# Performance work log

Hardware: AMD Instinct MI355X
Metric: run time of the kernel (lower is better)

Reference implementation:

```python
import jax, jax.numpy as jnp
import numpy as np

DIM = 768
NUM_HEADS = 12
HEAD_DIM = DIM // NUM_HEADS
SCALE = HEAD_DIM ** -0.5


def setup_inputs() -> dict:
    key = jax.random.key(0)
    k_x, k_qkv, k_proj, k_pb = jax.random.split(key, 4)
    B, N = 8, 1024
    x = jax.random.normal(k_x, (B, N, DIM), dtype=jnp.float32)
    # nn.Linear(dim, 3*dim, bias=False): weight [3*dim, dim]
    w_qkv = jax.random.normal(k_qkv, (3 * DIM, DIM), dtype=jnp.float32) * (DIM ** -0.5)
    # nn.Linear(dim, dim): weight [dim, dim], bias [dim]
    w_proj = jax.random.normal(k_proj, (DIM, DIM), dtype=jnp.float32) * (DIM ** -0.5)
    b_proj = jax.random.normal(k_pb, (DIM,), dtype=jnp.float32) * 0.01
    return {"x": x, "w_qkv": w_qkv, "w_proj": w_proj, "b_proj": b_proj}


def reference(x, w_qkv, w_proj, b_proj):
    B, N, C = x.shape
    H, D = NUM_HEADS, HEAD_DIM
    # qkv: [B, N, 3C] -> [3, B, H, N, D]
    qkv = jnp.einsum('bnc,oc->bno', x, w_qkv)
    qkv = qkv.reshape(B, N, 3, H, D).transpose(2, 0, 3, 1, 4)
    q, k, v = qkv[0], qkv[1], qkv[2]
    # scores in float32 (module explicitly casts to float)
    attn = jnp.einsum('bhnd,bhmd->bhnm', q.astype(jnp.float32), k.astype(jnp.float32)) * SCALE
    attn = jax.nn.softmax(attn, axis=-1)
    attn = jnp.where(jnp.isnan(attn), 0.0, attn)  # masked_fill nan -> 0
    out = jnp.einsum('bhnm,bhmd->bhnd', attn, v.astype(jnp.float32))
    out = out.transpose(0, 2, 1, 3).reshape(B, N, C)
    out = jnp.einsum('bnc,oc->bno', out, w_proj) + b_proj
    return out
```

## Files before the change

kernel.cpp:

```cpp
#include <hip/hip_runtime.h>

typedef _Float16 half8 __attribute__((ext_vector_type(8)));
typedef _Float16 half4 __attribute__((ext_vector_type(4)));
typedef float f32x4 __attribute__((ext_vector_type(4)));

#define NHEAD 12
#define HDIM  64
#define SEQ   1024
#define CDIM  768
#define O3    2304
#define MTOK  8192

__device__ __forceinline__ void load_lds16(const void* g, void* l) {
  __builtin_amdgcn_global_load_lds(
      (const __attribute__((address_space(1))) unsigned int*)g,
      (__attribute__((address_space(3))) unsigned int*)l, 16, 0, 0);
}

__global__ __launch_bounds__(256) void cast_f2h(const float* __restrict__ in,
                                                _Float16* __restrict__ out) {
  size_t i = ((size_t)blockIdx.x * 256 + threadIdx.x) * 4;
  float4 v = *reinterpret_cast<const float4*>(in + i);
  half4 h;
  h[0] = (_Float16)v.x; h[1] = (_Float16)v.y; h[2] = (_Float16)v.z; h[3] = (_Float16)v.w;
  *reinterpret_cast<half4*>(out + i) = h;
}

__global__ __launch_bounds__(256) void qkv_gemm(const _Float16* __restrict__ A,
                                                const _Float16* __restrict__ Bw,
                                                _Float16* __restrict__ Qh,
                                                _Float16* __restrict__ Kh,
                                                _Float16* __restrict__ VT) {
  __shared__ _Float16 As0[128 * 64], Bs0[128 * 64];
  __shared__ _Float16 As1[128 * 64], Bs1[128 * 64];
  const int tid  = threadIdx.x;
  const int lane = tid & 63;
  const int wv   = tid >> 6;
  const int wm   = wv >> 1;
  const int wn   = wv & 1;
  const int fr   = lane & 15;
  const int kg   = lane >> 4;

  const int lin = blockIdx.y * gridDim.x + blockIdx.x;
  const int cpx = (gridDim.x * gridDim.y) >> 3;
  const int swz = (lin & 7) * cpx + (lin >> 3);
  const int m0  = (swz / 18) * 128;
  const int n0  = (swz % 18) * 128;

  f32x4 acc[4][4];
#pragma unroll
  for (int i = 0; i < 4; ++i)
#pragma unroll
    for (int j = 0; j < 4; ++j) acc[i][j] = (f32x4){0.f, 0.f, 0.f, 0.f};

  auto stage = [&](_Float16* Ad, _Float16* Bd, int kt) {
#pragma unroll
    for (int r = 0; r < 4; ++r) {
      const int c = r * 256 + tid;
      const int row = c >> 3, cc = c & 7;
      load_lds16(A + (size_t)(m0 + row) * CDIM + kt + ((cc ^ (row & 7)) * 8), Ad + c * 8);
    }
#pragma unroll
    for (int r = 0; r < 4; ++r) {
      const int c = r * 256 + tid;
      const int row = c >> 3, cc = c & 7;
      load_lds16(Bw + (size_t)(n0 + row) * CDIM + kt + ((cc ^ (row & 7)) * 8), Bd + c * 8);
    }
  };

  auto compute = [&](const _Float16* As, const _Float16* Bs) {
#pragma unroll
    for (int kk = 0; kk < 2; ++kk) {
      half8 a[4], b[4];
#pragma unroll
      for (int i = 0; i < 4; ++i) {
        const int row = wm * 64 + i * 16 + fr;
        a[i] = *reinterpret_cast<const half8*>(
            &As[row * 64 + (((kk * 4 + kg) ^ (row & 7)) * 8)]);
      }
#pragma unroll
      for (int j = 0; j < 4; ++j) {
        const int row = wn * 64 + j * 16 + fr;
        b[j] = *reinterpret_cast<const half8*>(
            &Bs[row * 64 + (((kk * 4 + kg) ^ (row & 7)) * 8)]);
      }
#pragma unroll
      for (int i = 0; i < 4; ++i)
#pragma unroll
        for (int j = 0; j < 4; ++j)
          acc[i][j] = __builtin_amdgcn_mfma_f32_16x16x32_f16(a[i], b[j], acc[i][j], 0, 0, 0);
    }
  };

  stage(As0, Bs0, 0);
  __syncthreads();
  for (int it = 0; it < 6; ++it) {
    const int kt = it * 128;
    stage(As1, Bs1, kt + 64);
    compute(As0, Bs0);
    __syncthreads();
    if (kt + 128 < CDIM) stage(As0, Bs0, kt + 128);
    compute(As1, Bs1);
    __syncthreads();
  }

  const int t     = n0 / CDIM;
  const int hbase = n0 - t * CDIM;
#pragma unroll
  for (int i = 0; i < 4; ++i) {
    const int mrow = m0 + wm * 64 + i * 16 + kg * 4;
#pragma unroll
    for (int j = 0; j < 4; ++j) {
      const int hd = hbase + wn * 64 + j * 16 + fr;
      const int h  = hd >> 6, d = hd & 63;
#pragma unroll
      for (int r = 0; r < 4; ++r) {
        const int m  = mrow + r;
        const int bb = m >> 10, nn = m & 1023;
        const float v = acc[i][j][r];
        if (t == 0)
          Qh[(((size_t)(bb * NHEAD + h)) << 16) + (nn << 6) + d] = (_Float16)(v * 0.125f);
        else if (t == 1)
          Kh[(((size_t)(bb * NHEAD + h)) << 16) + (nn << 6) + d] = (_Float16)v;
        else
          VT[(((size_t)(bb * NHEAD + h)) << 16) + (d << 10) + nn] = (_Float16)v;
      }
    }
  }
}

__global__ __launch_bounds__(256) void attn_kernel(const _Float16* __restrict__ Qh,
                                                   const _Float16* __restrict__ Kh,
                                                   const _Float16* __restrict__ VT,
                                                   _Float16* __restrict__ AO) {
  __shared__ _Float16 Ks0[64 * 64], Vs0[64 * 64];
  __shared__ _Float16 Ks1[64 * 64], Vs1[64 * 64];
  __shared__ _Float16 Ps[4 * 16 * 64];
  const int tid  = threadIdx.x;
  const int lane = tid & 63;
  const int w    = tid >> 6;
  const int fr   = lane & 15;
  const int kg   = lane >> 4;
  const int kh   = kg * 8;
  const int bh   = blockIdx.x;
  const int qt   = blockIdx.y;
  const int q0   = qt * 64 + w * 16;
  const size_t qkbase = (size_t)bh * SEQ * HDIM;
  char* const psw = (char*)&Ps[w * 16 * 64];

  half8 qb[2];
#pragma unroll
  for (int ks = 0; ks < 2; ++ks)
    qb[ks] = *reinterpret_cast<const half8*>(
        &Qh[qkbase + (size_t)(q0 + fr) * HDIM + ks * 32 + kh]);

  f32x4 O[4];
  float mrun = -__builtin_inff();
  float lrun = 0.f;
#pragma unroll
  for (int fd = 0; fd < 4; ++fd) O[fd] = (f32x4){0.f, 0.f, 0.f, 0.f};

  auto stageKV = [&](_Float16* Kd, _Float16* Vd, int kt) {
#pragma unroll
    for (int r = 0; r < 2; ++r) {
      const int c = r * 256 + tid;
      const int row = c >> 3, cc = c & 7;
      load_lds16(&Kh[qkbase + (size_t)(kt + row) * HDIM + ((cc ^ (row & 7)) * 8)], Kd + c * 8);
    }
#pragma unroll
    for (int r = 0; r < 2; ++r) {
      const int c = r * 256 + tid;
      const int row = c >> 3, cc = c & 7;
      load_lds16(&VT[(size_t)bh * HDIM * SEQ + (size_t)row * SEQ + kt + ((cc ^ (row & 7)) * 8)],
                 Vd + c * 8);
    }
  };

  auto computeKV = [&](const _Float16* Ksrc, const _Float16* Vsrc) {
    f32x4 st[4];
#pragma unroll
    for (int fc = 0; fc < 4; ++fc) st[fc] = (f32x4){0.f, 0.f, 0.f, 0.f};
#pragma unroll
    for (int ks = 0; ks < 2; ++ks) {
#pragma unroll
      for (int fc = 0; fc < 4; ++fc) {
        const int row = fc * 16 + fr;
        const int colh = ks * 32 + kh;
        half8 ka = *reinterpret_cast<const half8*>(
            &Ksrc[row * 64 + (((colh >> 3) ^ (row & 7)) << 3)]);
        st[fc] = __builtin_amdgcn_mfma_f32_16x16x32_f16(ka, qb[ks], st[fc], 0, 0, 0);
      }
    }

    float mx = st[0][0];
#pragma unroll
    for (int fc = 0; fc < 4; ++fc)
#pragma unroll
      for (int r = 0; r < 4; ++r) mx = fmaxf(mx, st[fc][r]);
    mx = fmaxf(mx, __shfl_xor(mx, 16));
    mx = fmaxf(mx, __shfl_xor(mx, 32));
    const float mnew = fmaxf(mrun, mx);
    const float corr = __expf(mrun - mnew);
    mrun = mnew;
    float rs = 0.f;
#pragma unroll
    for (int fc = 0; fc < 4; ++fc)
#pragma unroll
      for (int r = 0; r < 4; ++r) {
        const float p = __expf(st[fc][r] - mnew);
        st[fc][r] = p;
        rs += p;
      }
    rs += __shfl_xor(rs, 16);
    rs += __shfl_xor(rs, 32);
    lrun = lrun * corr + rs;

#pragma unroll
    for (int r = 0; r < 4; ++r) {
      const float c4 = __shfl(corr, kg * 4 + r);
#pragma unroll
      for (int fd = 0; fd < 4; ++fd) O[fd][r] *= c4;
    }

#pragma unroll
    for (int fc = 0; fc < 4; ++fc) {
      half4 pk;
      pk[0] = (_Float16)st[fc][0];
      pk[1] = (_Float16)st[fc][1];
      pk[2] = (_Float16)st[fc][2];
      pk[3] = (_Float16)st[fc][3];
      const int slot = (fc * 2 + (kg >> 1)) ^ (fr & 7);
      *reinterpret_cast<half4*>(psw + fr * 128 + slot * 16 + (kg & 1) * 8) = pk;
    }

#pragma unroll
    for (int ks = 0; ks < 2; ++ks) {
      const int rslot = (ks * 4 + kg) ^ (fr & 7);
      half8 pa = *reinterpret_cast<half8*>(psw + fr * 128 + rslot * 16);
#pragma unroll
      for (int fd = 0; fd < 4; ++fd) {
        const int row = fd * 16 + fr;
        const int colh = ks * 32 + kh;
        half8 vb = *reinterpret_cast<const half8*>(
            &Vsrc[row * 64 + (((colh >> 3) ^ (row & 7)) << 3)]);
        O[fd] = __builtin_amdgcn_mfma_f32_16x16x32_f16(pa, vb, O[fd], 0, 0, 0);
      }
    }
  };

  stageKV(Ks0, Vs0, 0);
  __syncthreads();
  for (int it = 0; it < 8; ++it) {
    const int kt = it * 128;
    stageKV(Ks1, Vs1, kt + 64);
    computeKV(Ks0, Vs0);
    __syncthreads();
    if (kt + 128 < SEQ) stageKV(Ks0, Vs0, kt + 128);
    computeKV(Ks1, Vs1);
    __syncthreads();
  }

  const int b = bh / NHEAD, h = bh % NHEAD;
  const float linv = 1.0f / lrun;
#pragma unroll
  for (int r = 0; r < 4; ++r) {
    const float lq = __shfl(linv, kg * 4 + r);
    const int n = q0 + kg * 4 + r;
#pragma unroll
    for (int fd = 0; fd < 4; ++fd)
      AO[((size_t)b * SEQ + n) * CDIM + h * HDIM + fd * 16 + fr] =
          (_Float16)(O[fd][r] * lq);
  }
}

__global__ __launch_bounds__(256) void proj_gemm(const _Float16* __restrict__ A,
                                                 const _Float16* __restrict__ Bw,
                                                 const float* __restrict__ bias,
                                                 float* __restrict__ Out) {
  __shared__ _Float16 As0[128 * 64], Bs0[128 * 64];
  __shared__ _Float16 As1[128 * 64], Bs1[128 * 64];
  const int tid  = threadIdx.x;
  const int lane = tid & 63;
  const int wv   = tid >> 6;
  const int wm   = wv >> 1;
  const int wn   = wv & 1;
  const int fr   = lane & 15;
  const int kg   = lane >> 4;

  const int lin = blockIdx.y * gridDim.x + blockIdx.x;
  const int cpx = (gridDim.x * gridDim.y) >> 3;
  const int swz = (lin & 7) * cpx + (lin >> 3);
  const int m0  = (swz / 6) * 128;
  const int n0  = (swz % 6) * 128;

  f32x4 acc[4][4];
#pragma unroll
  for (int i = 0; i < 4; ++i)
#pragma unroll
    for (int j = 0; j < 4; ++j) acc[i][j] = (f32x4){0.f, 0.f, 0.f, 0.f};

  auto stage = [&](_Float16* Ad, _Float16* Bd, int kt) {
#pragma unroll
    for (int r = 0; r < 4; ++r) {
      const int c = r * 256 + tid;
      const int row = c >> 3, cc = c & 7;
      load_lds16(A + (size_t)(m0 + row) * CDIM + kt + ((cc ^ (row & 7)) * 8), Ad + c * 8);
    }
#pragma unroll
    for (int r = 0; r < 4; ++r) {
      const int c = r * 256 + tid;
      const int row = c >> 3, cc = c & 7;
      load_lds16(Bw + (size_t)(n0 + row) * CDIM + kt + ((cc ^ (row & 7)) * 8), Bd + c * 8);
    }
  };

  auto compute = [&](const _Float16* As, const _Float16* Bs) {
#pragma unroll
    for (int kk = 0; kk < 2; ++kk) {
      half8 a[4], b[4];
#pragma unroll
      for (int i = 0; i < 4; ++i) {
        const int row = wm * 64 + i * 16 + fr;
        a[i] = *reinterpret_cast<const half8*>(
            &As[row * 64 + (((kk * 4 + kg) ^ (row & 7)) * 8)]);
      }
#pragma unroll
      for (int j = 0; j < 4; ++j) {
        const int row = wn * 64 + j * 16 + fr;
        b[j] = *reinterpret_cast<const half8*>(
            &Bs[row * 64 + (((kk * 4 + kg) ^ (row & 7)) * 8)]);
      }
#pragma unroll
      for (int i = 0; i < 4; ++i)
#pragma unroll
        for (int j = 0; j < 4; ++j)
          acc[i][j] = __builtin_amdgcn_mfma_f32_16x16x32_f16(a[i], b[j], acc[i][j], 0, 0, 0);
    }
  };

  stage(As0, Bs0, 0);
  __syncthreads();
  for (int it = 0; it < 6; ++it) {
    const int kt = it * 128;
    stage(As1, Bs1, kt + 64);
    compute(As0, Bs0);
    __syncthreads();
    if (kt + 128 < CDIM) stage(As0, Bs0, kt + 128);
    compute(As1, Bs1);
    __syncthreads();
  }

#pragma unroll
  for (int i = 0; i < 4; ++i) {
    const int mrow = m0 + wm * 64 + i * 16 + kg * 4;
#pragma unroll
    for (int j = 0; j < 4; ++j) {
      const int ocol = n0 + wn * 64 + j * 16 + fr;
      const float bv = bias[ocol];
#pragma unroll
      for (int r = 0; r < 4; ++r)
        Out[(size_t)(mrow + r) * CDIM + ocol] = acc[i][j][r] + bv;
    }
  }
}

extern "C" void kernel_launch(void* const* d_in, const int* in_sizes, int n_in,
                              void* d_out, int out_size, void* d_ws, size_t ws_size,
                              hipStream_t stream) {
  const float* x     = (const float*)d_in[0];
  const float* wqkv  = (const float*)d_in[1];
  const float* wproj = (const float*)d_in[2];
  const float* bproj = (const float*)d_in[3];
  float* out = (float*)d_out;

  char* ws = (char*)d_ws;
  _Float16* x_h     = (_Float16*)(ws);
  _Float16* wqkv_h  = (_Float16*)(ws + 12582912);
  _Float16* wproj_h = (_Float16*)(ws + 16121856);
  _Float16* Qh      = (_Float16*)(ws + 17301504);
  _Float16* Kh      = (_Float16*)(ws + 29884416);
  _Float16* VT      = (_Float16*)(ws + 42467328);
  _Float16* AOh     = (_Float16*)(ws + 55050240);

  cast_f2h<<<6291456 / 1024, 256, 0, stream>>>(x, x_h);
  cast_f2h<<<1769472 / 1024, 256, 0, stream>>>(wqkv, wqkv_h);
  cast_f2h<<<589824 / 1024, 256, 0, stream>>>(wproj, wproj_h);

  qkv_gemm<<<dim3(O3 / 128, MTOK / 128), 256, 0, stream>>>(x_h, wqkv_h, Qh, Kh, VT);
  attn_kernel<<<dim3(96, 16), 256, 0, stream>>>(Qh, Kh, VT, AOh);
  proj_gemm<<<dim3(CDIM / 128, MTOK / 128), 256, 0, stream>>>(AOh, wproj_h, bproj, out);
}
```

Baseline: 144.0 us.

## Enlarge attention query tile, add lazy softmax rescale, exp2 scaling, new GEMM swizzle

The attention kernel now runs 512 threads per block covering 128 queries, so each staged K/V tile is shared by eight waves and each thread issues a single load per tile. Q is pre-scaled by log2(e) so softmax can use exp2f. The running-max rescale of O and l is skipped unless some row's max has grown by more than 8, which trades exactness of the reference max for fewer shuffles and multiplies and leaves some risk of fp16 range issues. Both GEMMs also get a new block-to-tile mapping meant to improve L2 locality across the XCDs.

After: 136.6 us. 5.2% less time.

```diff
diff --git a/kernel.cpp b/kernel.cpp
--- a/kernel.cpp
+++ b/kernel.cpp
@@ -42,16 +42,16 @@
   const int kg   = lane >> 4;
 
   const int lin = blockIdx.y * gridDim.x + blockIdx.x;
-  const int cpx = (gridDim.x * gridDim.y) >> 3;
-  const int swz = (lin & 7) * cpx + (lin >> 3);
-  const int m0  = (swz / 18) * 128;
-  const int n0  = (swz % 18) * 128;
+  const int k   = lin & 7;
+  const int j   = lin >> 3;
+  const int n0  = (j >> 3) * 128;
+  const int m0  = (k * 8 + (j & 7)) * 128;
 
   f32x4 acc[4][4];
 #pragma unroll
   for (int i = 0; i < 4; ++i)
 #pragma unroll
-    for (int j = 0; j < 4; ++j) acc[i][j] = (f32x4){0.f, 0.f, 0.f, 0.f};
+    for (int j2 = 0; j2 < 4; ++j2) acc[i][j2] = (f32x4){0.f, 0.f, 0.f, 0.f};
 
   auto stage = [&](_Float16* Ad, _Float16* Bd, int kt) {
 #pragma unroll
@@ -79,16 +79,16 @@
             &As[row * 64 + (((kk * 4 + kg) ^ (row & 7)) * 8)]);
       }
 #pragma unroll
-      for (int j = 0; j < 4; ++j) {
-        const int row = wn * 64 + j * 16 + fr;
-        b[j] = *reinterpret_cast<const half8*>(
+      for (int j2 = 0; j2 < 4; ++j2) {
+        const int row = wn * 64 + j2 * 16 + fr;
+        b[j2] = *reinterpret_cast<const half8*>(
             &Bs[row * 64 + (((kk * 4 + kg) ^ (row & 7)) * 8)]);
       }
 #pragma unroll
       for (int i = 0; i < 4; ++i)
 #pragma unroll
-        for (int j = 0; j < 4; ++j)
-          acc[i][j] = __builtin_amdgcn_mfma_f32_16x16x32_f16(a[i], b[j], acc[i][j], 0, 0, 0);
+        for (int j2 = 0; j2 < 4; ++j2)
+          acc[i][j2] = __builtin_amdgcn_mfma_f32_16x16x32_f16(a[i], b[j2], acc[i][j2], 0, 0, 0);
     }
   };
 
@@ -104,22 +104,23 @@
     __syncthreads();
   }
 
+  const float QSCALE = 0.125f * 1.44269504088896f;
   const int t     = n0 / CDIM;
   const int hbase = n0 - t * CDIM;
 #pragma unroll
   for (int i = 0; i < 4; ++i) {
     const int mrow = m0 + wm * 64 + i * 16 + kg * 4;
 #pragma unroll
-    for (int j = 0; j < 4; ++j) {
-      const int hd = hbase + wn * 64 + j * 16 + fr;
+    for (int j2 = 0; j2 < 4; ++j2) {
+      const int hd = hbase + wn * 64 + j2 * 16 + fr;
       const int h  = hd >> 6, d = hd & 63;
 #pragma unroll
       for (int r = 0; r < 4; ++r) {
         const int m  = mrow + r;
         const int bb = m >> 10, nn = m & 1023;
-        const float v = acc[i][j][r];
+        const float v = acc[i][j2][r];
         if (t == 0)
-          Qh[(((size_t)(bb * NHEAD + h)) << 16) + (nn << 6) + d] = (_Float16)(v * 0.125f);
+          Qh[(((size_t)(bb * NHEAD + h)) << 16) + (nn << 6) + d] = (_Float16)(v * QSCALE);
         else if (t == 1)
           Kh[(((size_t)(bb * NHEAD + h)) << 16) + (nn << 6) + d] = (_Float16)v;
         else
@@ -129,13 +130,13 @@
   }
 }
 
-__global__ __launch_bounds__(256) void attn_kernel(const _Float16* __restrict__ Qh,
+__global__ __launch_bounds__(512) void attn_kernel(const _Float16* __restrict__ Qh,
                                                    const _Float16* __restrict__ Kh,
                                                    const _Float16* __restrict__ VT,
                                                    _Float16* __restrict__ AO) {
   __shared__ _Float16 Ks0[64 * 64], Vs0[64 * 64];
   __shared__ _Float16 Ks1[64 * 64], Vs1[64 * 64];
-  __shared__ _Float16 Ps[4 * 16 * 64];
+  __shared__ _Float16 Ps[8 * 16 * 64];
   const int tid  = threadIdx.x;
   const int lane = tid & 63;
   const int w    = tid >> 6;
@@ -144,7 +145,7 @@
   const int kh   = kg * 8;
   const int bh   = blockIdx.x;
   const int qt   = blockIdx.y;
-  const int q0   = qt * 64 + w * 16;
+  const int q0   = qt * 128 + w * 16;
   const size_t qkbase = (size_t)bh * SEQ * HDIM;
   char* const psw = (char*)&Ps[w * 16 * 64];
 
@@ -161,19 +162,11 @@
   for (int fd = 0; fd < 4; ++fd) O[fd] = (f32x4){0.f, 0.f, 0.f, 0.f};
 
   auto stageKV = [&](_Float16* Kd, _Float16* Vd, int kt) {
-#pragma unroll
-    for (int r = 0; r < 2; ++r) {
-      const int c = r * 256 + tid;
-      const int row = c >> 3, cc = c & 7;
-      load_lds16(&Kh[qkbase + (size_t)(kt + row) * HDIM + ((cc ^ (row & 7)) * 8)], Kd + c * 8);
-    }
-#pragma unroll
-    for (int r = 0; r < 2; ++r) {
-      const int c = r * 256 + tid;
-      const int row = c >> 3, cc = c & 7;
-      load_lds16(&VT[(size_t)bh * HDIM * SEQ + (size_t)row * SEQ + kt + ((cc ^ (row & 7)) * 8)],
-                 Vd + c * 8);
-    }
+    const int c = tid;
+    const int row = c >> 3, cc = c & 7;
+    load_lds16(&Kh[qkbase + (size_t)(kt + row) * HDIM + ((cc ^ (row & 7)) * 8)], Kd + c * 8);
+    load_lds16(&VT[(size_t)bh * HDIM * SEQ + (size_t)row * SEQ + kt + ((cc ^ (row & 7)) * 8)],
+               Vd + c * 8);
   };
 
   auto computeKV = [&](const _Float16* Ksrc, const _Float16* Vsrc) {
@@ -199,28 +192,32 @@
       for (int r = 0; r < 4; ++r) mx = fmaxf(mx, st[fc][r]);
     mx = fmaxf(mx, __shfl_xor(mx, 16));
     mx = fmaxf(mx, __shfl_xor(mx, 32));
-    const float mnew = fmaxf(mrun, mx);
-    const float corr = __expf(mrun - mnew);
-    mrun = mnew;
+
+    if (!__all(mx - mrun <= 8.f)) {
+      const float mnew = fmaxf(mrun, mx);
+      const float corr = exp2f(mrun - mnew);
+      mrun = mnew;
+      lrun *= corr;
+#pragma unroll
+      for (int r = 0; r < 4; ++r) {
+        const float c4 = __shfl(corr, kg * 4 + r);
+#pragma unroll
+        for (int fd = 0; fd < 4; ++fd) O[fd][r] *= c4;
+      }
+    }
+
     float rs = 0.f;
 #pragma unroll
     for (int fc = 0; fc < 4; ++fc)
 #pragma unroll
       for (int r = 0; r < 4; ++r) {
-        const float p = __expf(st[fc][r] - mnew);
+        const float p = exp2f(st[fc][r] - mrun);
         st[fc][r] = p;
         rs += p;
       }
     rs += __shfl_xor(rs, 16);
     rs += __shfl_xor(rs, 32);
-    lrun = lrun * corr + rs;
-
-#pragma unroll
-    for (int r = 0; r < 4; ++r) {
-      const float c4 = __shfl(corr, kg * 4 + r);
-#pragma unroll
-      for (int fd = 0; fd < 4; ++fd) O[fd][r] *= c4;
-    }
+    lrun += rs;
 
 #pragma unroll
     for (int fc = 0; fc < 4; ++fc) {
@@ -288,16 +285,16 @@
   const int kg   = lane >> 4;
 
   const int lin = blockIdx.y * gridDim.x + blockIdx.x;
-  const int cpx = (gridDim.x * gridDim.y) >> 3;
-  const int swz = (lin & 7) * cpx + (lin >> 3);
-  const int m0  = (swz / 6) * 128;
-  const int n0  = (swz % 6) * 128;
+  const int k   = lin & 7;
+  const int j   = lin >> 3;
+  const int n0  = (j >> 3) * 128;
+  const int m0  = (k * 8 + (j & 7)) * 128;
 
   f32x4 acc[4][4];
 #pragma unroll
   for (int i = 0; i < 4; ++i)
 #pragma unroll
-    for (int j = 0; j < 4; ++j) acc[i][j] = (f32x4){0.f, 0.f, 0.f, 0.f};
+    for (int j2 = 0; j2 < 4; ++j2) acc[i][j2] = (f32x4){0.f, 0.f, 0.f, 0.f};
 
   auto stage = [&](_Float16* Ad, _Float16* Bd, int kt) {
 #pragma unroll
@@ -325,16 +322,16 @@
             &As[row * 64 + (((kk * 4 + kg) ^ (row & 7)) * 8)]);
       }
 #pragma unroll
-      for (int j = 0; j < 4; ++j) {
-        const int row = wn * 64 + j * 16 + fr;
-        b[j] = *reinterpret_cast<const half8*>(
+      for (int j2 = 0; j2 < 4; ++j2) {
+        const int row = wn * 64 + j2 * 16 + fr;
+        b[j2] = *reinterpret_cast<const half8*>(
             &Bs[row * 64 + (((kk * 4 + kg) ^ (row & 7)) * 8)]);
       }
 #pragma unroll
       for (int i = 0; i < 4; ++i)
 #pragma unroll
-        for (int j = 0; j < 4; ++j)
-          acc[i][j] = __builtin_amdgcn_mfma_f32_16x16x32_f16(a[i], b[j], acc[i][j], 0, 0, 0);
+        for (int j2 = 0; j2 < 4; ++j2)
+          acc[i][j2] = __builtin_amdgcn_mfma_f32_16x16x32_f16(a[i], b[j2], acc[i][j2], 0, 0, 0);
     }
   };
 
@@ -354,12 +351,12 @@
   for (int i = 0; i < 4; ++i) {
     const int mrow = m0 + wm * 64 + i * 16 + kg * 4;
 #pragma unroll
-    for (int j = 0; j < 4; ++j) {
-      const int ocol = n0 + wn * 64 + j * 16 + fr;
+    for (int j2 = 0; j2 < 4; ++j2) {
+      const int ocol = n0 + wn * 64 + j2 * 16 + fr;
       const float bv = bias[ocol];
 #pragma unroll
       for (int r = 0; r < 4; ++r)
-        Out[(size_t)(mrow + r) * CDIM + ocol] = acc[i][j][r] + bv;
+        Out[(size_t)(mrow + r) * CDIM + ocol] = acc[i][j2][r] + bv;
     }
   }
 }
@@ -387,6 +384,6 @@
   cast_f2h<<<589824 / 1024, 256, 0, stream>>>(wproj, wproj_h);
 
   qkv_gemm<<<dim3(O3 / 128, MTOK / 128), 256, 0, stream>>>(x_h, wqkv_h, Qh, Kh, VT);
-  attn_kernel<<<dim3(96, 16), 256, 0, stream>>>(Qh, Kh, VT, AOh);
+  attn_kernel<<<dim3(96, 8), 512, 0, stream>>>(Qh, Kh, VT, AOh);
   proj_gemm<<<dim3(CDIM / 128, MTOK / 128), 256, 0, stream>>>(AOh, wproj_h, bproj, out);
 }
```

## Triple-buffer GEMMs and attention with 512-thread blocks and lazy softmax rescaling

Applied to the files above, without the earlier changes.

Both GEMMs move to 256x128 tiles with 512 threads and a three-stage LDS ring using explicit vmcnt waits and a single barrier per k-step, plus setprio around the MFMA blocks. Attention handles 128 queries per block with a three-buffer K/V ring. Q is prescaled by log2(e) so the softmax can use exp2f, and the running max is only rescaled when it grows by more than a threshold. The aim is to cut barrier overhead and memory stalls and to reduce exp and rescale work, at the cost of more LDS per block, fewer blocks per CU, and reliance on hand-placed waitcnt counts being correct.

Result: no change. 142.8 us (-0.8%).

```diff
diff --git a/kernel.cpp b/kernel.cpp
--- a/kernel.cpp
+++ b/kernel.cpp
@@ -26,13 +26,14 @@
   *reinterpret_cast<half4*>(out + i) = h;
 }
 
-__global__ __launch_bounds__(256) void qkv_gemm(const _Float16* __restrict__ A,
+
+__global__ __launch_bounds__(512) void qkv_gemm(const _Float16* __restrict__ A,
                                                 const _Float16* __restrict__ Bw,
                                                 _Float16* __restrict__ Qh,
                                                 _Float16* __restrict__ Kh,
                                                 _Float16* __restrict__ VT) {
-  __shared__ _Float16 As0[128 * 64], Bs0[128 * 64];
-  __shared__ _Float16 As1[128 * 64], Bs1[128 * 64];
+  __shared__ _Float16 Ab[3][256 * 64];
+  __shared__ _Float16 Bb[3][128 * 64];
   const int tid  = threadIdx.x;
   const int lane = tid & 63;
   const int wv   = tid >> 6;
@@ -41,11 +42,11 @@
   const int fr   = lane & 15;
   const int kg   = lane >> 4;
 
-  const int lin = blockIdx.y * gridDim.x + blockIdx.x;
-  const int cpx = (gridDim.x * gridDim.y) >> 3;
-  const int swz = (lin & 7) * cpx + (lin >> 3);
-  const int m0  = (swz / 18) * 128;
-  const int n0  = (swz % 18) * 128;
+  const int lin = blockIdx.x;
+  const int xk  = lin & 7;
+  const int xj  = lin >> 3;
+  const int m0  = (xk * 4 + (xj & 3)) * 256;
+  const int n0  = (xj >> 2) * 128;
 
   f32x4 acc[4][4];
 #pragma unroll
@@ -53,22 +54,22 @@
 #pragma unroll
     for (int j = 0; j < 4; ++j) acc[i][j] = (f32x4){0.f, 0.f, 0.f, 0.f};
 
-  auto stage = [&](_Float16* Ad, _Float16* Bd, int kt) {
+  auto stageT = [&](int bi, int kt) {
 #pragma unroll
     for (int r = 0; r < 4; ++r) {
-      const int c = r * 256 + tid;
+      const int c = r * 512 + tid;
       const int row = c >> 3, cc = c & 7;
-      load_lds16(A + (size_t)(m0 + row) * CDIM + kt + ((cc ^ (row & 7)) * 8), Ad + c * 8);
-    }
-#pragma unroll
-    for (int r = 0; r < 4; ++r) {
-      const int c = r * 256 + tid;
+      load_lds16(A + (size_t)(m0 + row) * CDIM + kt + ((cc ^ (row & 7)) * 8), &Ab[bi][c * 8]);
+    }
+#pragma unroll
+    for (int r = 0; r < 2; ++r) {
+      const int c = r * 512 + tid;
       const int row = c >> 3, cc = c & 7;
-      load_lds16(Bw + (size_t)(n0 + row) * CDIM + kt + ((cc ^ (row & 7)) * 8), Bd + c * 8);
-    }
-  };
-
-  auto compute = [&](const _Float16* As, const _Float16* Bs) {
+      load_lds16(Bw + (size_t)(n0 + row) * CDIM + kt + ((cc ^ (row & 7)) * 8), &Bb[bi][c * 8]);
+    }
+  };
+
+  auto computeT = [&](int bi) {
 #pragma unroll
     for (int kk = 0; kk < 2; ++kk) {
       half8 a[4], b[4];
@@ -76,36 +77,40 @@
       for (int i = 0; i < 4; ++i) {
         const int row = wm * 64 + i * 16 + fr;
         a[i] = *reinterpret_cast<const half8*>(
-            &As[row * 64 + (((kk * 4 + kg) ^ (row & 7)) * 8)]);
+            &Ab[bi][row * 64 + (((kk * 4 + kg) ^ (row & 7)) * 8)]);
       }
 #pragma unroll
       for (int j = 0; j < 4; ++j) {
         const int row = wn * 64 + j * 16 + fr;
         b[j] = *reinterpret_cast<const half8*>(
-            &Bs[row * 64 + (((kk * 4 + kg) ^ (row & 7)) * 8)]);
-      }
+            &Bb[bi][row * 64 + (((kk * 4 + kg) ^ (row & 7)) * 8)]);
+      }
+      __builtin_amdgcn_s_setprio(1);
 #pragma unroll
       for (int i = 0; i < 4; ++i)
 #pragma unroll
         for (int j = 0; j < 4; ++j)
           acc[i][j] = __builtin_amdgcn_mfma_f32_16x16x32_f16(a[i], b[j], acc[i][j], 0, 0, 0);
-    }
-  };
-
-  stage(As0, Bs0, 0);
-  __syncthreads();
-  for (int it = 0; it < 6; ++it) {
-    const int kt = it * 128;
-    stage(As1, Bs1, kt + 64);
-    compute(As0, Bs0);
-    __syncthreads();
-    if (kt + 128 < CDIM) stage(As0, Bs0, kt + 128);
-    compute(As1, Bs1);
-    __syncthreads();
-  }
-
-  const int t     = n0 / CDIM;
-  const int hbase = n0 - t * CDIM;
+      __builtin_amdgcn_s_setprio(0);
+    }
+  };
+
+  stageT(0, 0);
+  stageT(1, 64);
+#pragma unroll
+  for (int t = 0; t < 12; ++t) {
+    if (t + 1 < 12) { asm volatile("s_waitcnt vmcnt(6)" ::: "memory"); }
+    else            { asm volatile("s_waitcnt vmcnt(0)" ::: "memory"); }
+    __builtin_amdgcn_s_barrier();
+    __builtin_amdgcn_sched_barrier(0);
+    if (t + 2 < 12) stageT((t + 2) % 3, (t + 2) * 64);
+    computeT(t % 3);
+    __builtin_amdgcn_sched_barrier(0);
+  }
+
+  const float QSCALE = 0.125f * 1.44269504088896f;
+  const int t0    = n0 / CDIM;
+  const int hbase = n0 - t0 * CDIM;
 #pragma unroll
   for (int i = 0; i < 4; ++i) {
     const int mrow = m0 + wm * 64 + i * 16 + kg * 4;
@@ -118,9 +123,9 @@
         const int m  = mrow + r;
         const int bb = m >> 10, nn = m & 1023;
         const float v = acc[i][j][r];
-        if (t == 0)
-          Qh[(((size_t)(bb * NHEAD + h)) << 16) + (nn << 6) + d] = (_Float16)(v * 0.125f);
-        else if (t == 1)
+        if (t0 == 0)
+          Qh[(((size_t)(bb * NHEAD + h)) << 16) + (nn << 6) + d] = (_Float16)(v * QSCALE);
+        else if (t0 == 1)
           Kh[(((size_t)(bb * NHEAD + h)) << 16) + (nn << 6) + d] = (_Float16)v;
         else
           VT[(((size_t)(bb * NHEAD + h)) << 16) + (d << 10) + nn] = (_Float16)v;
@@ -129,13 +134,13 @@
   }
 }
 
-__global__ __launch_bounds__(256) void attn_kernel(const _Float16* __restrict__ Qh,
+__global__ __launch_bounds__(512) void attn_kernel(const _Float16* __restrict__ Qh,
                                                    const _Float16* __restrict__ Kh,
                                                    const _Float16* __restrict__ VT,
                                                    _Float16* __restrict__ AO) {
-  __shared__ _Float16 Ks0[64 * 64], Vs0[64 * 64];
-  __shared__ _Float16 Ks1[64 * 64], Vs1[64 * 64];
-  __shared__ _Float16 Ps[4 * 16 * 64];
+  __shared__ _Float16 Ks[3][64 * 64];
+  __shared__ _Float16 Vs[3][64 * 64];
+  __shared__ _Float16 Ps[8 * 16 * 64];
   const int tid  = threadIdx.x;
   const int lane = tid & 63;
   const int w    = tid >> 6;
@@ -144,7 +149,7 @@
   const int kh   = kg * 8;
   const int bh   = blockIdx.x;
   const int qt   = blockIdx.y;
-  const int q0   = qt * 64 + w * 16;
+  const int q0   = qt * 128 + w * 16;
   const size_t qkbase = (size_t)bh * SEQ * HDIM;
   char* const psw = (char*)&Ps[w * 16 * 64];
 
@@ -160,20 +165,13 @@
 #pragma unroll
   for (int fd = 0; fd < 4; ++fd) O[fd] = (f32x4){0.f, 0.f, 0.f, 0.f};
 
-  auto stageKV = [&](_Float16* Kd, _Float16* Vd, int kt) {
-#pragma unroll
-    for (int r = 0; r < 2; ++r) {
-      const int c = r * 256 + tid;
-      const int row = c >> 3, cc = c & 7;
-      load_lds16(&Kh[qkbase + (size_t)(kt + row) * HDIM + ((cc ^ (row & 7)) * 8)], Kd + c * 8);
-    }
-#pragma unroll
-    for (int r = 0; r < 2; ++r) {
-      const int c = r * 256 + tid;
-      const int row = c >> 3, cc = c & 7;
-      load_lds16(&VT[(size_t)bh * HDIM * SEQ + (size_t)row * SEQ + kt + ((cc ^ (row & 7)) * 8)],
-                 Vd + c * 8);
-    }
+  auto stageKV = [&](int bi, int t) {
+    const int kt = t * 64;
+    const int row = tid >> 3, cc = tid & 7;
+    load_lds16(&Kh[qkbase + (size_t)(kt + row) * HDIM + ((cc ^ (row & 7)) * 8)],
+               &Ks[bi][tid * 8]);
+    load_lds16(&VT[(size_t)bh * HDIM * SEQ + (size_t)row * SEQ + kt + ((cc ^ (row & 7)) * 8)],
+               &Vs[bi][tid * 8]);
   };
 
   auto computeKV = [&](const _Float16* Ksrc, const _Float16* Vsrc) {
@@ -199,28 +197,32 @@
       for (int r = 0; r < 4; ++r) mx = fmaxf(mx, st[fc][r]);
     mx = fmaxf(mx, __shfl_xor(mx, 16));
     mx = fmaxf(mx, __shfl_xor(mx, 32));
-    const float mnew = fmaxf(mrun, mx);
-    const float corr = __expf(mrun - mnew);
-    mrun = mnew;
+
+    if (!__all(mx - mrun <= 8.f)) {
+      const float mnew = fmaxf(mrun, mx);
+      const float corr = exp2f(mrun - mnew);
+      mrun = mnew;
+      lrun *= corr;
+#pragma unroll
+      for (int r = 0; r < 4; ++r) {
+        const float c4 = __shfl(corr, kg * 4 + r);
+#pragma unroll
+        for (int fd = 0; fd < 4; ++fd) O[fd][r] *= c4;
+      }
+    }
+
     float rs = 0.f;
 #pragma unroll
     for (int fc = 0; fc < 4; ++fc)
 #pragma unroll
       for (int r = 0; r < 4; ++r) {
-        const float p = __expf(st[fc][r] - mnew);
+        const float p = exp2f(st[fc][r] - mrun);
         st[fc][r] = p;
         rs += p;
       }
     rs += __shfl_xor(rs, 16);
     rs += __shfl_xor(rs, 32);
-    lrun = lrun * corr + rs;
-
-#pragma unroll
-    for (int r = 0; r < 4; ++r) {
-      const float c4 = __shfl(corr, kg * 4 + r);
-#pragma unroll
-      for (int fd = 0; fd < 4; ++fd) O[fd][r] *= c4;
-    }
+    lrun += rs;
 
 #pragma unroll
     for (int fc = 0; fc < 4; ++fc) {
@@ -248,16 +250,16 @@
     }
   };
 
-  stageKV(Ks0, Vs0, 0);
-  __syncthreads();
-  for (int it = 0; it < 8; ++it) {
-    const int kt = it * 128;
-    stageKV(Ks1, Vs1, kt + 64);
-    computeKV(Ks0, Vs0);
-    __syncthreads();
-    if (kt + 128 < SEQ) stageKV(Ks0, Vs0, kt + 128);
-    computeKV(Ks1, Vs1);
-    __syncthreads();
+  stageKV(0, 0);
+  stageKV(1, 1);
+#pragma unroll
+  for (int t = 0; t < 16; ++t) {
+    if (t + 1 < 16) { asm volatile("s_waitcnt vmcnt(2)" ::: "memory"); }
+    else            { asm volatile("s_waitcnt vmcnt(0)" ::: "memory"); }
+    __builtin_amdgcn_s_barrier();
+    __builtin_amdgcn_sched_barrier(0);
+    if (t + 2 < 16) stageKV((t + 2) % 3, t + 2);
+    computeKV(&Ks[t % 3][0], &Vs[t % 3][0]);
   }
 
   const int b = bh / NHEAD, h = bh % NHEAD;
@@ -273,12 +275,12 @@
   }
 }
 
-__global__ __launch_bounds__(256) void proj_gemm(const _Float16* __restrict__ A,
+__global__ __launch_bounds__(512) void proj_gemm(const _Float16* __restrict__ A,
                                                  const _Float16* __restrict__ Bw,
                                                  const float* __restrict__ bias,
                                                  float* __restrict__ Out) {
-  __shared__ _Float16 As0[128 * 64], Bs0[128 * 64];
-  __shared__ _Float16 As1[128 * 64], Bs1[128 * 64];
+  __shared__ _Float16 Ab[3][256 * 64];
+  __shared__ _Float16 Bb[3][128 * 64];
   const int tid  = threadIdx.x;
   const int lane = tid & 63;
   const int wv   = tid >> 6;
@@ -287,11 +289,11 @@
   const int fr   = lane & 15;
   const int kg   = lane >> 4;
 
-  const int lin = blockIdx.y * gridDim.x + blockIdx.x;
-  const int cpx = (gridDim.x * gridDim.y) >> 3;
-  const int swz = (lin & 7) * cpx + (lin >> 3);
-  const int m0  = (swz / 6) * 128;
-  const int n0  = (swz % 6) * 128;
+  const int lin = blockIdx.x;
+  const int xk  = lin & 7;
+  const int xj  = lin >> 3;
+  const int m0  = (xk * 4 + (xj & 3)) * 256;
+  const int n0  = (xj >> 2) * 128;
 
   f32x4 acc[4][4];
 #pragma unroll
@@ -299,22 +301,22 @@
 #pragma unroll
     for (int j = 0; j < 4; ++j) acc[i][j] = (f32x4){0.f, 0.f, 0.f, 0.f};
 
-  auto stage = [&](_Float16* Ad, _Float16* Bd, int kt) {
+  auto stageT = [&](int bi, int kt) {
 #pragma unroll
     for (int r = 0; r < 4; ++r) {
-      const int c = r * 256 + tid;
+      const int c = r * 512 + tid;
       const int row = c >> 3, cc = c & 7;
-      load_lds16(A + (size_t)(m0 + row) * CDIM + kt + ((cc ^ (row & 7)) * 8), Ad + c * 8);
-    }
-#pragma unroll
-    for (int r = 0; r < 4; ++r) {
-      const int c = r * 256 + tid;
+      load_lds16(A + (size_t)(m0 + row) * CDIM + kt + ((cc ^ (row & 7)) * 8), &Ab[bi][c * 8]);
+    }
+#pragma unroll
+    for (int r = 0; r < 2; ++r) {
+      const int c = r * 512 + tid;
       const int row = c >> 3, cc = c & 7;
-      load_lds16(Bw + (size_t)(n0 + row) * CDIM + kt + ((cc ^ (row & 7)) * 8), Bd + c * 8);
-    }
-  };
-
-  auto compute = [&](const _Float16* As, const _Float16* Bs) {
+      load_lds16(Bw + (size_t)(n0 + row) * CDIM + kt + ((cc ^ (row & 7)) * 8), &Bb[bi][c * 8]);
+    }
+  };
+
+  auto computeT = [&](int bi) {
 #pragma unroll
     for (int kk = 0; kk < 2; ++kk) {
       half8 a[4], b[4];
@@ -322,32 +324,35 @@
       for (int i = 0; i < 4; ++i) {
         const int row = wm * 64 + i * 16 + fr;
         a[i] = *reinterpret_cast<const half8*>(
-            &As[row * 64 + (((kk * 4 + kg) ^ (row & 7)) * 8)]);
+            &Ab[bi][row * 64 + (((kk * 4 + kg) ^ (row & 7)) * 8)]);
       }
 #pragma unroll
       for (int j = 0; j < 4; ++j) {
         const int row = wn * 64 + j * 16 + fr;
         b[j] = *reinterpret_cast<const half8*>(
-            &Bs[row * 64 + (((kk * 4 + kg) ^ (row & 7)) * 8)]);
-      }
+            &Bb[bi][row * 64 + (((kk * 4 + kg) ^ (row & 7)) * 8)]);
+      }
+      __builtin_amdgcn_s_setprio(1);
 #pragma unroll
       for (int i = 0; i < 4; ++i)
 #pragma unroll
         for (int j = 0; j < 4; ++j)
           acc[i][j] = __builtin_amdgcn_mfma_f32_16x16x32_f16(a[i], b[j], acc[i][j], 0, 0, 0);
-    }
-  };
-
-  stage(As0, Bs0, 0);
-  __syncthreads();
-  for (int it = 0; it < 6; ++it) {
-    const int kt = it * 128;
-    stage(As1, Bs1, kt + 64);
-    compute(As0, Bs0);
-    __syncthreads();
-    if (kt + 128 < CDIM) stage(As0, Bs0, kt + 128);
-    compute(As1, Bs1);
-    __syncthreads();
+      __builtin_amdgcn_s_setprio(0);
+    }
+  };
+
+  stageT(0, 0);
+  stageT(1, 64);
+#pragma unroll
+  for (int t = 0; t < 12; ++t) {
+    if (t + 1 < 12) { asm volatile("s_waitcnt vmcnt(6)" ::: "memory"); }
+    else            { asm volatile("s_waitcnt vmcnt(0)" ::: "memory"); }
+    __builtin_amdgcn_s_barrier();
+    __builtin_amdgcn_sched_barrier(0);
+    if (t + 2 < 12) stageT((t + 2) % 3, (t + 2) * 64);
+    computeT(t % 3);
+    __builtin_amdgcn_sched_barrier(0);
   }
 
 #pragma unroll
@@ -386,7 +391,7 @@
   cast_f2h<<<1769472 / 1024, 256, 0, stream>>>(wqkv, wqkv_h);
   cast_f2h<<<589824 / 1024, 256, 0, stream>>>(wproj, wproj_h);
 
-  qkv_gemm<<<dim3(O3 / 128, MTOK / 128), 256, 0, stream>>>(x_h, wqkv_h, Qh, Kh, VT);
-  attn_kernel<<<dim3(96, 16), 256, 0, stream>>>(Qh, Kh, VT, AOh);
-  proj_gemm<<<dim3(CDIM / 128, MTOK / 128), 256, 0, stream>>>(AOh, wproj_h, bproj, out);
-}
+  qkv_gemm<<<576, 512, 0, stream>>>(x_h, wqkv_h, Qh, Kh, VT);
+  attn_kernel<<<dim3(96, 8), 512, 0, stream>>>(Qh, Kh, VT, AOh);
+  proj_gemm<<<192, 512, 0, stream>>>(AOh, wproj_h, bproj, out);
+}
```
